# Kernel optimization log

Hardware: AMD Instinct MI355X
Metric: run time of the kernel (lower is better)

## Reference

```python
import jax, jax.numpy as jnp
import numpy as np

N, E, H, HEADS, NC, BLK = 100000, 1600000, 128, 4, 8192, 128

def _layernorm(x, g, b, eps=1e-5):
    m = jnp.mean(x, axis=-1, keepdims=True)
    v = jnp.var(x, axis=-1, keepdims=True)
    return (x - m) * jax.lax.rsqrt(v + eps) * g + b

def setup_inputs() -> dict:
    key = jax.random.key(0)
    ks = jax.random.split(key, 24)
    s = 0.05
    p = lambda k, shp: jax.random.normal(k, shp, jnp.float32) * s
    return {
        'x': jax.random.normal(ks[0], (N, H), jnp.float32),
        'ea': jax.random.normal(ks[1], (E, H), jnp.float32),
        # GINEConv edge linear (edge_dim -> hidden)
        'We': p(ks[2], (H, H)), 'be_': p(ks[3], (H,)),
        # GINEConv mlp: Linear(H,H) -> ReLU -> Linear(H,H)
        'W1': p(ks[4], (H, H)), 'b1': p(ks[5], (H,)),
        'W2': p(ks[6], (H, H)), 'b2': p(ks[7], (H,)),
        'ln1_g': jnp.ones((H,), jnp.float32), 'ln1_b': jnp.zeros((H,), jnp.float32),
        # MultiheadAttention packed qkv + out proj
        'in_w': p(ks[8], (3 * H, H)), 'in_b': p(ks[9], (3 * H,)),
        'out_w': p(ks[10], (H, H)), 'out_b': p(ks[11], (H,)),
        'ln2_g': jnp.ones((H,), jnp.float32), 'ln2_b': jnp.zeros((H,), jnp.float32),
        # FFN: Linear(H,2H) -> ReLU -> Linear(2H,H)
        'f1_w': p(ks[12], (2 * H, H)), 'f1_b': p(ks[13], (2 * H,)),
        'f2_w': p(ks[14], (H, 2 * H)), 'f2_b': p(ks[15], (H,)),
        'ei': jax.random.randint(ks[16], (2, E), 0, N, jnp.int64),
        'chem_idx': jnp.arange(NC, dtype=jnp.int64),
        'B': BLK,
    }

def reference(x, ea, We, be_, W1, b1, W2, b2, ln1_g, ln1_b, in_w, in_b,
              out_w, out_b, ln2_g, ln2_b, f1_w, f1_b, f2_w, f2_b,
              ei, chem_idx, B):
    n = x.shape[0]
    # ---- GINEConv: out_i = mlp((1+eps)*x_i + sum_j relu(x_j + lin(e_ji))), eps=0 ----
    src, dst = ei[0], ei[1]
    msg = jax.nn.relu(x[src] + ea @ We.T + be_)          # [E, H]
    agg = jax.ops.segment_sum(msg, dst, num_segments=n)  # [N, H]
    h = agg + x
    h = jax.nn.relu(h @ W1.T + b1) @ W2.T + b2
    x = _layernorm(x + h, ln1_g, ln1_b)
    # ---- chunked self-attention over chem nodes (chunks of size B) ----
    xc = x[chem_idx].reshape(-1, B, x.shape[-1])         # [nc, B, H]
    nc, _, hid = xc.shape
    dh = hid // HEADS
    qkv = xc @ in_w.T + in_b                             # [nc, B, 3H]
    q, k, v = jnp.split(qkv, 3, axis=-1)
    sp = lambda t: t.reshape(nc, B, HEADS, dh)
    att = jax.nn.softmax(jnp.einsum('bqhd,bkhd->bhqk', sp(q), sp(k)) * (1.0 / np.sqrt(dh)).astype(np.float32), axis=-1)
    o = jnp.einsum('bhqk,bkhd->bqhd', att, sp(v)).reshape(nc, B, hid)
    xc = xc + (o @ out_w.T + out_b)                      # residual inside BlockMHA
    xc = xc.reshape(-1, hid)
    # ---- FFN on chem subset ----
    h2 = _layernorm(xc, ln2_g, ln2_b)
    xc = xc + (jax.nn.relu(h2 @ f1_w.T + f1_b) @ f2_w.T + f2_b)
    return x.at[chem_idx].set(xc)
```

## Files before the change

### kernel.cpp

```cpp
#include <hip/hip_runtime.h>
#include <hip/hip_bf16.h>
#include <math.h>

typedef __attribute__((ext_vector_type(8))) __bf16 bf16x8;
typedef __attribute__((ext_vector_type(4))) float f32x4;
typedef __attribute__((ext_vector_type(4))) unsigned short u16x4;

#define HD  128
#define LDP 136

__device__ __forceinline__ unsigned short f2bf(float f) {
  __bf16 h = (__bf16)f;
  union { __bf16 h; unsigned short u; } v; v.h = h; return v.u;
}
__device__ __forceinline__ float bf2f(unsigned short h) {
  union { unsigned u; float f; } v; v.u = ((unsigned)h) << 16; return v.f;
}

__device__ __forceinline__ int idx_at(const void* p, long long i, int is64) {
  if (is64) return (int)((const long long*)p)[i];
  return ((const int*)p)[i];
}

__device__ __forceinline__ void mfma_tile_128(const unsigned short* a_s,
                                              const unsigned short* w_s,
                                              int w, int l15, int lg,
                                              f32x4 acc[2][8]) {
#pragma unroll
  for (int kk = 0; kk < 4; ++kk) {
    bf16x8 a[2], b[8];
#pragma unroll
    for (int mt = 0; mt < 2; ++mt)
      a[mt] = *(const bf16x8*)&a_s[(w * 32 + mt * 16 + l15) * LDP + kk * 32 + lg * 8];
#pragma unroll
    for (int nt = 0; nt < 8; ++nt)
      b[nt] = *(const bf16x8*)&w_s[(nt * 16 + l15) * LDP + kk * 32 + lg * 8];
#pragma unroll
    for (int mt = 0; mt < 2; ++mt)
#pragma unroll
      for (int nt = 0; nt < 8; ++nt)
        acc[mt][nt] = __builtin_amdgcn_mfma_f32_16x16x32_bf16(a[mt], b[nt], acc[mt][nt], 0, 0, 0);
  }
}

__device__ __forceinline__ void stage_f32(unsigned short* dst, const float* src,
                                          long long src_ld, int tid) {
  for (int i = tid; i < 128 * 32; i += 256) {
    int r = i >> 5, c = (i & 31) << 2;
    float4 f = *(const float4*)&src[(long long)r * src_ld + c];
    u16x4 h = { f2bf(f.x), f2bf(f.y), f2bf(f.z), f2bf(f.w) };
    *(u16x4*)&dst[r * LDP + c] = h;
  }
}

__global__ void detect_idx_kernel(const void* __restrict__ ei, int E, int N,
                                  int* __restrict__ flag) {
  if (threadIdx.x == 0 && blockIdx.x == 0) {
    const long long* p = (const long long*)ei;
    int is64 = 1;
    long long step = E / 64; if (step < 1) step = 1;
    for (int i = 0; i < 64; ++i) {
      long long v = p[i * step];
      if (v < 0 || v >= N) { is64 = 0; break; }
    }
    *flag = is64;
  }
}

__global__ __launch_bounds__(256) void hist_kernel(const void* __restrict__ ei,
                                                   const int* __restrict__ flag,
                                                   int* __restrict__ deg, int E) {
  const int is64 = *flag;
  for (long long e = blockIdx.x * 256LL + threadIdx.x; e < E;
       e += (long long)gridDim.x * 256)
    atomicAdd(&deg[idx_at(ei, (long long)E + e, is64)], 1);
}

#define SCH 1024
__global__ __launch_bounds__(256) void scan_a(const int* __restrict__ deg,
                                              int* __restrict__ bsum, int N) {
  const int b = blockIdx.x, t = threadIdx.x;
  int p = 0;
#pragma unroll
  for (int k = 0; k < 4; ++k) {
    int idx = b * SCH + t * 4 + k;
    if (idx < N) p += deg[idx];
  }
  __shared__ int warr[4];
  for (int o = 32; o > 0; o >>= 1) p += __shfl_xor(p, o);
  if ((t & 63) == 0) warr[t >> 6] = p;
  __syncthreads();
  if (t == 0) bsum[b] = warr[0] + warr[1] + warr[2] + warr[3];
}
__global__ void scan_b(int* __restrict__ bsum, int* __restrict__ off, int NB, int N) {
  if (threadIdx.x == 0 && blockIdx.x == 0) {
    int run = 0;
    for (int b = 0; b < NB; ++b) { int t = bsum[b]; bsum[b] = run; run += t; }
    off[N] = run;
  }
}
__global__ __launch_bounds__(256) void scan_c(const int* __restrict__ deg,
                                              const int* __restrict__ bsum,
                                              int* __restrict__ off,
                                              int* __restrict__ cursor, int N) {
  const int b = blockIdx.x, t = threadIdx.x;
  int d[4], s = 0;
#pragma unroll
  for (int k = 0; k < 4; ++k) {
    int idx = b * SCH + t * 4 + k;
    d[k] = (idx < N) ? deg[idx] : 0;
    s += d[k];
  }
  __shared__ int arr[256];
  arr[t] = s;
  __syncthreads();
  for (int stp = 1; stp < 256; stp <<= 1) {
    int v = (t >= stp) ? arr[t - stp] : 0;
    __syncthreads();
    arr[t] += v;
    __syncthreads();
  }
  int base = bsum[b] + arr[t] - s;
  int acc = 0;
#pragma unroll
  for (int k = 0; k < 4; ++k) {
    int idx = b * SCH + t * 4 + k;
    if (idx < N) { off[idx] = base + acc; cursor[idx] = base + acc; }
    acc += d[k];
  }
}

__global__ __launch_bounds__(256, 3) void edge_kernel4(
    const float* __restrict__ x, const float* __restrict__ ea,
    const float* __restrict__ We, const float* __restrict__ be,
    const void* __restrict__ ei, const int* __restrict__ flag,
    int* __restrict__ cursor, unsigned short* __restrict__ msg, int E, int N) {
  __shared__ unsigned short we_s[128 * LDP];
  __shared__ int s_src[128];
  __shared__ int s_pos[128];
  const int tid = threadIdx.x;
  const long long e0 = (long long)blockIdx.x * 128;
  const int is64 = *flag;

  if (tid < 128) {
    long long e = e0 + tid;
    int s = 0, p = 0;
    if (e < E) {
      s = idx_at(ei, e, is64);
      int d = idx_at(ei, (long long)E + e, is64);
      p = atomicAdd(&cursor[d], 1);
    }
    s_src[tid] = s; s_pos[tid] = p;
  }

  const int lane = tid & 63, w = tid >> 6;
  const int l15 = lane & 15, lg = lane >> 4;

  float4 af[2][4][2];
#pragma unroll
  for (int mt = 0; mt < 2; ++mt) {
    long long row = e0 + w * 32 + mt * 16 + l15;
    const float* src = &ea[(row < E ? row : e0) * HD + lg * 8];
#pragma unroll
    for (int kk = 0; kk < 4; ++kk) {
      af[mt][kk][0] = *(const float4*)&src[kk * 32];
      af[mt][kk][1] = *(const float4*)&src[kk * 32 + 4];
    }
  }

  for (int i = tid; i < 128 * 32; i += 256) {
    int r = i >> 5, c = (i & 31) << 2;
    float4 g = *(const float4*)&We[r * HD + c];
    u16x4 hw = { f2bf(g.x), f2bf(g.y), f2bf(g.z), f2bf(g.w) };
    *(u16x4*)&we_s[r * LDP + c] = hw;
  }

  bf16x8 a[2][4];
#pragma unroll
  for (int mt = 0; mt < 2; ++mt)
#pragma unroll
    for (int kk = 0; kk < 4; ++kk) {
      float4 f0 = af[mt][kk][0], f1 = af[mt][kk][1];
      bf16x8 t;
      t[0] = (__bf16)f0.x; t[1] = (__bf16)f0.y; t[2] = (__bf16)f0.z; t[3] = (__bf16)f0.w;
      t[4] = (__bf16)f1.x; t[5] = (__bf16)f1.y; t[6] = (__bf16)f1.z; t[7] = (__bf16)f1.w;
      a[mt][kk] = t;
    }
  __syncthreads();

  f32x4 acc[2][8];
#pragma unroll
  for (int mt = 0; mt < 2; ++mt)
#pragma unroll
    for (int nt = 0; nt < 8; ++nt) acc[mt][nt] = (f32x4){0.f, 0.f, 0.f, 0.f};

#pragma unroll
  for (int kk = 0; kk < 4; ++kk) {
    bf16x8 b[8];
#pragma unroll
    for (int nt = 0; nt < 8; ++nt)
      b[nt] = *(const bf16x8*)&we_s[(nt * 16 + l15) * LDP + kk * 32 + lg * 8];
#pragma unroll
    for (int mt = 0; mt < 2; ++mt)
#pragma unroll
      for (int nt = 0; nt < 8; ++nt)
        acc[mt][nt] = __builtin_amdgcn_mfma_f32_16x16x32_bf16(a[mt][kk], b[nt], acc[mt][nt], 0, 0, 0);
  }

  float bev[8];
#pragma unroll
  for (int nt = 0; nt < 8; ++nt) bev[nt] = be[nt * 16 + l15];
  __syncthreads();

#pragma unroll
  for (int mt = 0; mt < 2; ++mt) {
#pragma unroll
    for (int r = 0; r < 4; ++r) {
      int m = w * 32 + mt * 16 + lg * 4 + r;
      if (e0 + m >= E) continue;
      const float* xrow = x + (size_t)s_src[m] * HD;
#pragma unroll
      for (int nt = 0; nt < 8; ++nt) {
        int n = nt * 16 + l15;
        float val = acc[mt][nt][r] + bev[nt] + xrow[n];
        we_s[m * LDP + n] = f2bf(val > 0.f ? val : 0.f);
      }
    }
  }
  __syncthreads();
  for (int i = tid; i < 128 * 16; i += 256) {
    int r = i >> 4, sg = i & 15;
    if (e0 + r >= E) continue;
    *(float4*)&msg[(size_t)s_pos[r] * 128 + sg * 8] = *(const float4*)&we_s[r * LDP + sg * 8];
  }
}

__global__ __launch_bounds__(256) void node_kernel2(
    const float* __restrict__ x, float* __restrict__ xo,
    const int* __restrict__ off, const unsigned short* __restrict__ msg,
    const float* __restrict__ W1, const float* __restrict__ b1,
    const float* __restrict__ W2, const float* __restrict__ b2,
    const float* __restrict__ g1, const float* __restrict__ bt1, int N) {
  __shared__ char smem[2 * 128 * LDP * 2];
  unsigned short* a_s = (unsigned short*)smem;
  unsigned short* w_s = (unsigned short*)smem + 128 * LDP;
  float* y_s = (float*)smem;
  const int tid = threadIdx.x;
  const long long r0 = (long long)blockIdx.x * 128;

  const int grp = tid >> 4, li = tid & 15;
  for (int r = grp; r < 128; r += 16) {
    long long gr = r0 + r;
    float a8[8] = {0.f, 0.f, 0.f, 0.f, 0.f, 0.f, 0.f, 0.f};
    if (gr < N) {
      float4 x0 = *(const float4*)&x[(size_t)gr * HD + li * 8];
      float4 x1 = *(const float4*)&x[(size_t)gr * HD + li * 8 + 4];
      a8[0] = x0.x; a8[1] = x0.y; a8[2] = x0.z; a8[3] = x0.w;
      a8[4] = x1.x; a8[5] = x1.y; a8[6] = x1.z; a8[7] = x1.w;
      const int j0 = off[gr], j1 = off[gr + 1];
      int j = j0;
      for (; j + 1 < j1; j += 2) {
        const u16x4* p0 = (const u16x4*)&msg[(size_t)j * 128 + li * 8];
        const u16x4* p1 = (const u16x4*)&msg[(size_t)(j + 1) * 128 + li * 8];
        u16x4 v0 = p0[0], v1 = p0[1], v2 = p1[0], v3 = p1[1];
#pragma unroll
        for (int k = 0; k < 4; ++k) {
          a8[k]     += bf2f(v0[k]) + bf2f(v2[k]);
          a8[4 + k] += bf2f(v1[k]) + bf2f(v3[k]);
        }
      }
      if (j < j1) {
        const u16x4* p0 = (const u16x4*)&msg[(size_t)j * 128 + li * 8];
        u16x4 v0 = p0[0], v1 = p0[1];
#pragma unroll
        for (int k = 0; k < 4; ++k) { a8[k] += bf2f(v0[k]); a8[4 + k] += bf2f(v1[k]); }
      }
    }
    u16x4 h0 = { f2bf(a8[0]), f2bf(a8[1]), f2bf(a8[2]), f2bf(a8[3]) };
    u16x4 h1 = { f2bf(a8[4]), f2bf(a8[5]), f2bf(a8[6]), f2bf(a8[7]) };
    *(u16x4*)&a_s[r * LDP + li * 8] = h0;
    *(u16x4*)&a_s[r * LDP + li * 8 + 4] = h1;
  }
  stage_f32(w_s, W1, HD, tid);
  __syncthreads();

  const int lane = tid & 63, w = tid >> 6;
  const int l15 = lane & 15, lg = lane >> 4;
  f32x4 acc[2][8];
#pragma unroll
  for (int mt = 0; mt < 2; ++mt)
#pragma unroll
    for (int nt = 0; nt < 8; ++nt) acc[mt][nt] = (f32x4){0.f, 0.f, 0.f, 0.f};
  mfma_tile_128(a_s, w_s, w, l15, lg, acc);
  __syncthreads();

#pragma unroll
  for (int mt = 0; mt < 2; ++mt)
#pragma unroll
    for (int r = 0; r < 4; ++r) {
      int m = w * 32 + mt * 16 + lg * 4 + r;
#pragma unroll
      for (int nt = 0; nt < 8; ++nt) {
        int n = nt * 16 + l15;
        float t = acc[mt][nt][r] + b1[n];
        a_s[m * LDP + n] = f2bf(t > 0.f ? t : 0.f);
      }
    }
  stage_f32(w_s, W2, HD, tid);
  __syncthreads();

  f32x4 acc2[2][8];
#pragma unroll
  for (int mt = 0; mt < 2; ++mt)
#pragma unroll
    for (int nt = 0; nt < 8; ++nt) acc2[mt][nt] = (f32x4){0.f, 0.f, 0.f, 0.f};
  mfma_tile_128(a_s, w_s, w, l15, lg, acc2);
  __syncthreads();

#pragma unroll
  for (int mt = 0; mt < 2; ++mt)
#pragma unroll
    for (int r = 0; r < 4; ++r) {
      int m = w * 32 + mt * 16 + lg * 4 + r;
      if (r0 + m < N) {
#pragma unroll
        for (int nt = 0; nt < 8; ++nt) {
          int n = nt * 16 + l15;
          y_s[m * 132 + n] = x[(r0 + m) * HD + n] + acc2[mt][nt][r] + b2[n];
        }
      }
    }
  __syncthreads();

  for (int row = w; row < 128; row += 4) {
    if (r0 + row >= N) continue;
    float v1 = y_s[row * 132 + lane], v2 = y_s[row * 132 + 64 + lane];
    float s = v1 + v2, sq = v1 * v1 + v2 * v2;
    for (int o = 32; o > 0; o >>= 1) { s += __shfl_xor(s, o); sq += __shfl_xor(sq, o); }
    float mean = s * (1.f / 128.f);
    float var = sq * (1.f / 128.f) - mean * mean;
    float rs = rsqrtf(var + 1e-5f);
    xo[(r0 + row) * HD + lane]      = (v1 - mean) * rs * g1[lane] + bt1[lane];
    xo[(r0 + row) * HD + 64 + lane] = (v2 - mean) * rs * g1[lane + 64] + bt1[lane + 64];
  }
}

__global__ __launch_bounds__(256) void edge_kernel(
    const float* __restrict__ x, const float* __restrict__ ea,
    const float* __restrict__ We, const float* __restrict__ be,
    const void* __restrict__ ei, const int* __restrict__ flag,
    float* __restrict__ agg, int E, int N) {
  __shared__ unsigned short ea_s[128 * LDP];
  __shared__ unsigned short we_s[128 * LDP];
  __shared__ int s_src[128];
  __shared__ int s_dst[128];
  const int tid = threadIdx.x;
  const long long e0 = (long long)blockIdx.x * 128;
  const int is64 = *flag;
  if (tid < 128) {
    long long e = e0 + tid;
    int s = 0, d = 0;
    if (e < E) { s = idx_at(ei, e, is64); d = idx_at(ei, (long long)E + e, is64); }
    s_src[tid] = s; s_dst[tid] = d;
  }
  for (int i = tid; i < 128 * 32; i += 256) {
    int r = i >> 5, c = (i & 31) << 2;
    float4 f = {0.f, 0.f, 0.f, 0.f};
    if (e0 + r < E) f = *(const float4*)&ea[(e0 + r) * HD + c];
    u16x4 h = { f2bf(f.x), f2bf(f.y), f2bf(f.z), f2bf(f.w) };
    *(u16x4*)&ea_s[r * LDP + c] = h;
    float4 g = *(const float4*)&We[r * HD + c];
    u16x4 hw = { f2bf(g.x), f2bf(g.y), f2bf(g.z), f2bf(g.w) };
    *(u16x4*)&we_s[r * LDP + c] = hw;
  }
  __syncthreads();
  const int lane = tid & 63, w = tid >> 6;
  const int l15 = lane & 15, lg = lane >> 4;
  f32x4 acc[2][8];
#pragma unroll
  for (int mt = 0; mt < 2; ++mt)
#pragma unroll
    for (int nt = 0; nt < 8; ++nt) acc[mt][nt] = (f32x4){0.f, 0.f, 0.f, 0.f};
  mfma_tile_128(ea_s, we_s, w, l15, lg, acc);
  float bev[8];
#pragma unroll
  for (int nt = 0; nt < 8; ++nt) bev[nt] = be[nt * 16 + l15];
#pragma unroll
  for (int mt = 0; mt < 2; ++mt) {
#pragma unroll
    for (int r = 0; r < 4; ++r) {
      int m = w * 32 + mt * 16 + lg * 4 + r;
      if (e0 + m >= E) continue;
      const float* xrow = x + (size_t)s_src[m] * HD;
      float* arow = agg + (size_t)s_dst[m] * HD;
#pragma unroll
      for (int nt = 0; nt < 8; ++nt) {
        int n = nt * 16 + l15;
        float val = acc[mt][nt][r] + bev[nt] + xrow[n];
        if (val > 0.f) unsafeAtomicAdd(&arow[n], val);
      }
    }
  }
}

__global__ __launch_bounds__(256) void node_kernel(
    const float* __restrict__ x, float* xo,
    const float* __restrict__ W1, const float* __restrict__ b1,
    const float* __restrict__ W2, const float* __restrict__ b2,
    const float* __restrict__ g1, const float* __restrict__ bt1, int N) {
  __shared__ char smem[2 * 128 * LDP * 2];
  unsigned short* a_s = (unsigned short*)smem;
  unsigned short* w_s = (unsigned short*)smem + 128 * LDP;
  float* y_s = (float*)smem;
  const int tid = threadIdx.x;
  const long long r0 = (long long)blockIdx.x * 128;
  for (int i = tid; i < 128 * 32; i += 256) {
    int r = i >> 5, c = (i & 31) << 2;
    float4 f = {0.f, 0.f, 0.f, 0.f};
    if (r0 + r < N) {
      float4 xa = *(const float4*)&x[(r0 + r) * HD + c];
      float4 ag = *(const float4*)&xo[(r0 + r) * HD + c];
      f.x = xa.x + ag.x; f.y = xa.y + ag.y; f.z = xa.z + ag.z; f.w = xa.w + ag.w;
    }
    u16x4 h = { f2bf(f.x), f2bf(f.y), f2bf(f.z), f2bf(f.w) };
    *(u16x4*)&a_s[r * LDP + c] = h;
    float4 g = *(const float4*)&W1[r * HD + c];
    u16x4 hw = { f2bf(g.x), f2bf(g.y), f2bf(g.z), f2bf(g.w) };
    *(u16x4*)&w_s[r * LDP + c] = hw;
  }
  __syncthreads();
  const int lane = tid & 63, w = tid >> 6;
  const int l15 = lane & 15, lg = lane >> 4;
  f32x4 acc[2][8];
#pragma unroll
  for (int mt = 0; mt < 2; ++mt)
#pragma unroll
    for (int nt = 0; nt < 8; ++nt) acc[mt][nt] = (f32x4){0.f, 0.f, 0.f, 0.f};
  mfma_tile_128(a_s, w_s, w, l15, lg, acc);
  __syncthreads();
#pragma unroll
  for (int mt = 0; mt < 2; ++mt)
#pragma unroll
    for (int r = 0; r < 4; ++r) {
      int m = w * 32 + mt * 16 + lg * 4 + r;
#pragma unroll
      for (int nt = 0; nt < 8; ++nt) {
        int n = nt * 16 + l15;
        float t = acc[mt][nt][r] + b1[n];
        a_s[m * LDP + n] = f2bf(t > 0.f ? t : 0.f);
      }
    }
  stage_f32(w_s, W2, HD, tid);
  __syncthreads();
  f32x4 acc2[2][8];
#pragma unroll
  for (int mt = 0; mt < 2; ++mt)
#pragma unroll
    for (int nt = 0; nt < 8; ++nt) acc2[mt][nt] = (f32x4){0.f, 0.f, 0.f, 0.f};
  mfma_tile_128(a_s, w_s, w, l15, lg, acc2);
  __syncthreads();
#pragma unroll
  for (int mt = 0; mt < 2; ++mt)
#pragma unroll
    for (int r = 0; r < 4; ++r) {
      int m = w * 32 + mt * 16 + lg * 4 + r;
      if (r0 + m < N) {
#pragma unroll
        for (int nt = 0; nt < 8; ++nt) {
          int n = nt * 16 + l15;
          y_s[m * 132 + n] = x[(r0 + m) * HD + n] + acc2[mt][nt][r] + b2[n];
        }
      }
    }
  __syncthreads();
  for (int row = w; row < 128; row += 4) {
    if (r0 + row >= N) continue;
    float v1 = y_s[row * 132 + lane], v2 = y_s[row * 132 + 64 + lane];
    float s = v1 + v2, sq = v1 * v1 + v2 * v2;
    for (int o = 32; o > 0; o >>= 1) { s += __shfl_xor(s, o); sq += __shfl_xor(sq, o); }
    float mean = s * (1.f / 128.f);
    float var = sq * (1.f / 128.f) - mean * mean;
    float rs = rsqrtf(var + 1e-5f);
    xo[(r0 + row) * HD + lane]      = (v1 - mean) * rs * g1[lane] + bt1[lane];
    xo[(r0 + row) * HD + 64 + lane] = (v2 - mean) * rs * g1[lane + 64] + bt1[lane + 64];
  }
}

__global__ __launch_bounds__(256) void qkv_kernel(
    const float* __restrict__ xo, const float* __restrict__ in_w,
    const float* __restrict__ in_b, const void* __restrict__ chem,
    const int* __restrict__ flag, float* __restrict__ qkv) {
  __shared__ unsigned short a_s[128 * LDP];
  __shared__ unsigned short w_s[128 * LDP];
  __shared__ int s_row[128];
  const int tid = threadIdx.x;
  const int chunk = blockIdx.x, sec = blockIdx.y;
  const int is64 = *flag;
  if (tid < 128) s_row[tid] = idx_at(chem, (long long)chunk * 128 + tid, is64);
  __syncthreads();
  for (int i = tid; i < 128 * 32; i += 256) {
    int r = i >> 5, c = (i & 31) << 2;
    float4 f = *(const float4*)&xo[(size_t)s_row[r] * HD + c];
    u16x4 h = { f2bf(f.x), f2bf(f.y), f2bf(f.z), f2bf(f.w) };
    *(u16x4*)&a_s[r * LDP + c] = h;
    float4 g = *(const float4*)&in_w[(size_t)(sec * 128 + r) * HD + c];
    u16x4 hw = { f2bf(g.x), f2bf(g.y), f2bf(g.z), f2bf(g.w) };
    *(u16x4*)&w_s[r * LDP + c] = hw;
  }
  __syncthreads();
  const int lane = tid & 63, w = tid >> 6;
  const int l15 = lane & 15, lg = lane >> 4;
  f32x4 acc[2][8];
#pragma unroll
  for (int mt = 0; mt < 2; ++mt)
#pragma unroll
    for (int nt = 0; nt < 8; ++nt) acc[mt][nt] = (f32x4){0.f, 0.f, 0.f, 0.f};
  mfma_tile_128(a_s, w_s, w, l15, lg, acc);
#pragma unroll
  for (int mt = 0; mt < 2; ++mt)
#pragma unroll
    for (int r = 0; r < 4; ++r) {
      int m = w * 32 + mt * 16 + lg * 4 + r;
#pragma unroll
      for (int nt = 0; nt < 8; ++nt) {
        int n = nt * 16 + l15;
        qkv[(size_t)(chunk * 128 + m) * 384 + sec * 128 + n] = acc[mt][nt][r] + in_b[sec * 128 + n];
      }
    }
}

__global__ __launch_bounds__(128) void attn_kernel(const float* __restrict__ qkv,
                                                   float* __restrict__ o) {
  __shared__ float k_s[128 * 32];
  __shared__ float v_s[128 * 32];
  const int tid = threadIdx.x;
  const int chunk = blockIdx.x, h = blockIdx.y;
  const float scale = 0.1767766952966369f;
  for (int i = tid; i < 128 * 32; i += 128) {
    int r = i >> 5, d = i & 31;
    k_s[i] = qkv[(size_t)(chunk * 128 + r) * 384 + 128 + h * 32 + d];
    v_s[i] = qkv[(size_t)(chunk * 128 + r) * 384 + 256 + h * 32 + d];
  }
  float qr[32];
  const int m = tid;
#pragma unroll
  for (int d = 0; d < 32; ++d)
    qr[d] = qkv[(size_t)(chunk * 128 + m) * 384 + h * 32 + d] * scale;
  __syncthreads();
  float mx = -1e30f, sm = 0.f;
  for (int j = 0; j < 128; ++j) {
    float s = 0.f;
#pragma unroll
    for (int d = 0; d < 32; ++d) s += qr[d] * k_s[j * 32 + d];
    if (s > mx) { sm = sm * __expf(mx - s); mx = s; }
    sm += __expf(s - mx);
  }
  const float inv = 1.f / sm;
  float ov[32];
#pragma unroll
  for (int d = 0; d < 32; ++d) ov[d] = 0.f;
  for (int j = 0; j < 128; ++j) {
    float s = 0.f;
#pragma unroll
    for (int d = 0; d < 32; ++d) s += qr[d] * k_s[j * 32 + d];
    float p = __expf(s - mx) * inv;
#pragma unroll
    for (int d = 0; d < 32; ++d) ov[d] += p * v_s[j * 32 + d];
  }
#pragma unroll
  for (int d = 0; d < 32; ++d)
    o[(size_t)(chunk * 128 + m) * HD + h * 32 + d] = ov[d];
}

__global__ __launch_bounds__(256) void oproj_kernel(
    const float* __restrict__ xo, const float* __restrict__ o,
    const float* __restrict__ Wo, const float* __restrict__ bo,
    const float* __restrict__ g2, const float* __restrict__ bt2,
    const void* __restrict__ chem, const int* __restrict__ flag,
    float* __restrict__ xc2, unsigned short* __restrict__ h2b) {
  __shared__ char smem[2 * 128 * LDP * 2];
  unsigned short* a_s = (unsigned short*)smem;
  unsigned short* w_s = (unsigned short*)smem + 128 * LDP;
  float* y_s = (float*)smem;
  __shared__ int s_row[128];
  const int tid = threadIdx.x;
  const int chunk = blockIdx.x;
  const int is64 = *flag;
  if (tid < 128) s_row[tid] = idx_at(chem, (long long)chunk * 128 + tid, is64);
  stage_f32(a_s, o + (size_t)chunk * 128 * HD, HD, tid);
  stage_f32(w_s, Wo, HD, tid);
  __syncthreads();
  const int lane = tid & 63, w = tid >> 6;
  const int l15 = lane & 15, lg = lane >> 4;
  f32x4 acc[2][8];
#pragma unroll
  for (int mt = 0; mt < 2; ++mt)
#pragma unroll
    for (int nt = 0; nt < 8; ++nt) acc[mt][nt] = (f32x4){0.f, 0.f, 0.f, 0.f};
  mfma_tile_128(a_s, w_s, w, l15, lg, acc);
  __syncthreads();
#pragma unroll
  for (int mt = 0; mt < 2; ++mt)
#pragma unroll
    for (int r = 0; r < 4; ++r) {
      int m = w * 32 + mt * 16 + lg * 4 + r;
#pragma unroll
      for (int nt = 0; nt < 8; ++nt) {
        int n = nt * 16 + l15;
        y_s[m * 132 + n] = xo[(size_t)s_row[m] * HD + n] + acc[mt][nt][r] + bo[n];
      }
    }
  __syncthreads();
  for (int row = w; row < 128; row += 4) {
    float v1 = y_s[row * 132 + lane], v2 = y_s[row * 132 + 64 + lane];
    float s = v1 + v2, sq = v1 * v1 + v2 * v2;
    for (int o2 = 32; o2 > 0; o2 >>= 1) { s += __shfl_xor(s, o2); sq += __shfl_xor(sq, o2); }
    float mean = s * (1.f / 128.f);
    float var = sq * (1.f / 128.f) - mean * mean;
    float rs = rsqrtf(var + 1e-5f);
    size_t gi = (size_t)(chunk * 128 + row) * HD;
    xc2[gi + lane] = v1; xc2[gi + 64 + lane] = v2;
    h2b[gi + lane]      = f2bf((v1 - mean) * rs * g2[lane] + bt2[lane]);
    h2b[gi + 64 + lane] = f2bf((v2 - mean) * rs * g2[lane + 64] + bt2[lane + 64]);
  }
}

__global__ __launch_bounds__(256) void ffn1_kernel(
    const unsigned short* __restrict__ h2b, const float* __restrict__ f1w,
    const float* __restrict__ f1b, unsigned short* __restrict__ u) {
  __shared__ unsigned short a_s[128 * LDP];
  __shared__ unsigned short w_s[128 * LDP];
  const int tid = threadIdx.x;
  const int chunk = blockIdx.x, sec = blockIdx.y;
  for (int i = tid; i < 128 * 32; i += 256) {
    int r = i >> 5, c = (i & 31) << 2;
    *(u16x4*)&a_s[r * LDP + c] = *(const u16x4*)&h2b[(size_t)(chunk * 128 + r) * HD + c];
  }
  stage_f32(w_s, f1w + (size_t)sec * 128 * HD, HD, tid);
  __syncthreads();
  const int lane = tid & 63, w = tid >> 6;
  const int l15 = lane & 15, lg = lane >> 4;
  f32x4 acc[2][8];
#pragma unroll
  for (int mt = 0; mt < 2; ++mt)
#pragma unroll
    for (int nt = 0; nt < 8; ++nt) acc[mt][nt] = (f32x4){0.f, 0.f, 0.f, 0.f};
  mfma_tile_128(a_s, w_s, w, l15, lg, acc);
#pragma unroll
  for (int mt = 0; mt < 2; ++mt)
#pragma unroll
    for (int r = 0; r < 4; ++r) {
      int m = w * 32 + mt * 16 + lg * 4 + r;
#pragma unroll
      for (int nt = 0; nt < 8; ++nt) {
        int n = nt * 16 + l15;
        float t = acc[mt][nt][r] + f1b[sec * 128 + n];
        u[(size_t)(chunk * 128 + m) * 256 + sec * 128 + n] = f2bf(t > 0.f ? t : 0.f);
      }
    }
}

__global__ __launch_bounds__(256) void ffn2_kernel(
    const unsigned short* __restrict__ u, const float* __restrict__ f2w,
    const float* __restrict__ f2b, const float* __restrict__ xc2,
    const void* __restrict__ chem, const int* __restrict__ flag,
    float* __restrict__ out) {
  __shared__ unsigned short a_s[128 * LDP];
  __shared__ unsigned short w_s[128 * LDP];
  __shared__ int s_row[128];
  const int tid = threadIdx.x;
  const int chunk = blockIdx.x;
  const int is64 = *flag;
  if (tid < 128) s_row[tid] = idx_at(chem, (long long)chunk * 128 + tid, is64);
  const int lane = tid & 63, w = tid >> 6;
  const int l15 = lane & 15, lg = lane >> 4;
  f32x4 acc[2][8];
#pragma unroll
  for (int mt = 0; mt < 2; ++mt)
#pragma unroll
    for (int nt = 0; nt < 8; ++nt) acc[mt][nt] = (f32x4){0.f, 0.f, 0.f, 0.f};
  for (int half = 0; half < 2; ++half) {
    __syncthreads();
    for (int i = tid; i < 128 * 32; i += 256) {
      int r = i >> 5, c = (i & 31) << 2;
      *(u16x4*)&a_s[r * LDP + c] =
          *(const u16x4*)&u[(size_t)(chunk * 128 + r) * 256 + half * 128 + c];
      float4 g = *(const float4*)&f2w[(size_t)r * 256 + half * 128 + c];
      u16x4 hw = { f2bf(g.x), f2bf(g.y), f2bf(g.z), f2bf(g.w) };
      *(u16x4*)&w_s[r * LDP + c] = hw;
    }
    __syncthreads();
    mfma_tile_128(a_s, w_s, w, l15, lg, acc);
  }
#pragma unroll
  for (int mt = 0; mt < 2; ++mt)
#pragma unroll
    for (int r = 0; r < 4; ++r) {
      int m = w * 32 + mt * 16 + lg * 4 + r;
#pragma unroll
      for (int nt = 0; nt < 8; ++nt) {
        int n = nt * 16 + l15;
        float val = xc2[(size_t)(chunk * 128 + m) * HD + n] + acc[mt][nt][r] + f2b[n];
        out[(size_t)s_row[m] * HD + n] = val;
      }
    }
}

extern "C" void kernel_launch(void* const* d_in, const int* in_sizes, int n_in,
                              void* d_out, int out_size, void* d_ws, size_t ws_size,
                              hipStream_t stream) {
  const float* x    = (const float*)d_in[0];
  const float* ea   = (const float*)d_in[1];
  const float* We   = (const float*)d_in[2];
  const float* be   = (const float*)d_in[3];
  const float* W1   = (const float*)d_in[4];
  const float* b1   = (const float*)d_in[5];
  const float* W2   = (const float*)d_in[6];
  const float* b2   = (const float*)d_in[7];
  const float* g1   = (const float*)d_in[8];
  const float* bt1  = (const float*)d_in[9];
  const float* in_w = (const float*)d_in[10];
  const float* in_b = (const float*)d_in[11];
  const float* outw = (const float*)d_in[12];
  const float* outb = (const float*)d_in[13];
  const float* g2   = (const float*)d_in[14];
  const float* bt2  = (const float*)d_in[15];
  const float* f1w  = (const float*)d_in[16];
  const float* f1b  = (const float*)d_in[17];
  const float* f2w  = (const float*)d_in[18];
  const float* f2b  = (const float*)d_in[19];
  const void*  ei   = d_in[20];
  const void*  chem = d_in[21];
  const int N  = in_sizes[0] / HD;
  const int E  = in_sizes[1] / HD;
  const int NC = in_sizes[21];
  const int NB = (N + SCH - 1) / SCH;
  float* xo = (float*)d_out;

  char* ws = (char*)d_ws;
  size_t o = 0;
  auto alloc = [&](size_t bytes) { size_t p = o; o = (o + bytes + 255) & ~255ULL; return p; };
  size_t o_qkv  = alloc((size_t)NC * 384 * 4);
  size_t o_obuf = alloc((size_t)NC * 128 * 4);
  size_t o_xc2  = alloc((size_t)NC * 128 * 4);
  size_t o_h2b  = alloc((size_t)NC * 128 * 2);
  size_t o_ubuf = alloc((size_t)NC * 256 * 2);
  size_t o_flag = alloc(4);
  size_t o_deg  = alloc((size_t)N * 4);
  size_t o_off  = alloc((size_t)(N + 1) * 4);
  size_t o_cur  = alloc((size_t)N * 4);
  size_t o_bsum = alloc((size_t)NB * 4);
  size_t o_msg  = alloc((size_t)E * 128 * 2);
  size_t need = o;

  float*          qkv  = (float*)(ws + o_qkv);
  float*          obuf = (float*)(ws + o_obuf);
  float*          xc2  = (float*)(ws + o_xc2);
  unsigned short* h2b  = (unsigned short*)(ws + o_h2b);
  unsigned short* ubuf = (unsigned short*)(ws + o_ubuf);
  int*            flag = (int*)(ws + o_flag);
  int*            deg  = (int*)(ws + o_deg);
  int*            off  = (int*)(ws + o_off);
  int*            cur  = (int*)(ws + o_cur);
  int*            bsum = (int*)(ws + o_bsum);
  unsigned short* msg  = (unsigned short*)(ws + o_msg);

  detect_idx_kernel<<<1, 64, 0, stream>>>(ei, E, N, flag);

  if (ws_size >= need) {
    hipMemsetAsync(deg, 0, (size_t)N * 4, stream);
    hist_kernel<<<dim3(1024), 256, 0, stream>>>(ei, flag, deg, E);
    scan_a<<<dim3(NB), 256, 0, stream>>>(deg, bsum, N);
    scan_b<<<1, 64, 0, stream>>>(bsum, off, NB, N);
    scan_c<<<dim3(NB), 256, 0, stream>>>(deg, bsum, off, cur, N);
    edge_kernel4<<<dim3((E + 127) / 128), 256, 0, stream>>>(x, ea, We, be, ei, flag,
                                                            cur, msg, E, N);
    node_kernel2<<<dim3((N + 127) / 128), 256, 0, stream>>>(x, xo, off, msg, W1, b1,
                                                            W2, b2, g1, bt1, N);
  } else {
    hipMemsetAsync(xo, 0, (size_t)N * HD * sizeof(float), stream);
    edge_kernel<<<dim3((E + 127) / 128), 256, 0, stream>>>(x, ea, We, be, ei, flag, xo, E, N);
    node_kernel<<<dim3((N + 127) / 128), 256, 0, stream>>>(x, xo, W1, b1, W2, b2, g1, bt1, N);
  }

  const int ncs = NC / 128;
  qkv_kernel<<<dim3(ncs, 3), 256, 0, stream>>>(xo, in_w, in_b, chem, flag, qkv);
  attn_kernel<<<dim3(ncs, 4), 128, 0, stream>>>(qkv, obuf);
  oproj_kernel<<<dim3(ncs), 256, 0, stream>>>(xo, obuf, outw, outb, g2, bt2, chem, flag, xc2, h2b);
  ffn1_kernel<<<dim3(ncs, 2), 256, 0, stream>>>(h2b, f1w, f1b, ubuf);
  ffn2_kernel<<<dim3(ncs), 256, 0, stream>>>(ubuf, f2w, f2b, xc2, chem, flag, xo);
}
```

Baseline: 807.4 us.

## Replace bf16 message buffer with dst-sorted edge ids and segmented atomic aggregation

Removes the large per-edge bf16 message buffer and the CSR gather in node_kernel2. A new scatter kernel writes edge ids and destinations in destination-sorted order. The edge kernel then processes edges in that order and sums consecutive same-destination rows in registers before issuing float atomics into the aggregation buffer, which node_kernel then consumes. This avoids writing and re-reading the E x 128 message array, at the cost of gathered (non-contiguous) ea row reads, an extra scatter pass, and float atomics that make the summation order nondeterministic.

```diff
diff --git a/kernel.cpp b/kernel.cpp
--- a/kernel.cpp
+++ b/kernel.cpp
@@ -130,27 +130,41 @@
   }
 }
 
-__global__ __launch_bounds__(256, 3) void edge_kernel4(
+__global__ __launch_bounds__(256) void scatter_eid_kernel(
+    const void* __restrict__ ei, const int* __restrict__ flag,
+    int* __restrict__ cursor, int* __restrict__ eid, int* __restrict__ dstc, int E) {
+  const int is64 = *flag;
+  for (long long e = blockIdx.x * 256LL + threadIdx.x; e < E;
+       e += (long long)gridDim.x * 256) {
+    int d = idx_at(ei, (long long)E + e, is64);
+    int pos = atomicAdd(&cursor[d], 1);
+    eid[pos] = (int)e;
+    dstc[pos] = d;
+  }
+}
+
+__global__ __launch_bounds__(256, 3) void edge_kernel5(
     const float* __restrict__ x, const float* __restrict__ ea,
     const float* __restrict__ We, const float* __restrict__ be,
     const void* __restrict__ ei, const int* __restrict__ flag,
-    int* __restrict__ cursor, unsigned short* __restrict__ msg, int E, int N) {
+    const int* __restrict__ eid, const int* __restrict__ dstc,
+    float* __restrict__ agg, int E) {
   __shared__ unsigned short we_s[128 * LDP];
   __shared__ int s_src[128];
-  __shared__ int s_pos[128];
+  __shared__ int s_dst[128];
   const int tid = threadIdx.x;
-  const long long e0 = (long long)blockIdx.x * 128;
+  const long long j0 = (long long)blockIdx.x * 128;
   const int is64 = *flag;
 
   if (tid < 128) {
-    long long e = e0 + tid;
-    int s = 0, p = 0;
-    if (e < E) {
-      s = idx_at(ei, e, is64);
-      int d = idx_at(ei, (long long)E + e, is64);
-      p = atomicAdd(&cursor[d], 1);
-    }
-    s_src[tid] = s; s_pos[tid] = p;
+    long long j = j0 + tid;
+    int srcv = 0, d = -1;
+    if (j < E) {
+      int e = eid[j];
+      srcv = idx_at(ei, e, is64);
+      d = dstc[j];
+    }
+    s_src[tid] = srcv; s_dst[tid] = d;
   }
 
   const int lane = tid & 63, w = tid >> 6;
@@ -159,8 +173,9 @@
   float4 af[2][4][2];
 #pragma unroll
   for (int mt = 0; mt < 2; ++mt) {
-    long long row = e0 + w * 32 + mt * 16 + l15;
-    const float* src = &ea[(row < E ? row : e0) * HD + lg * 8];
+    long long j = j0 + w * 32 + mt * 16 + l15;
+    int e = (j < E) ? eid[j] : 0;
+    const float* src = &ea[(size_t)e * HD + lg * 8];
 #pragma unroll
     for (int kk = 0; kk < 4; ++kk) {
       af[mt][kk][0] = *(const float4*)&src[kk * 32];
@@ -210,138 +225,42 @@
   float bev[8];
 #pragma unroll
   for (int nt = 0; nt < 8; ++nt) bev[nt] = be[nt * 16 + l15];
-  __syncthreads();
 
 #pragma unroll
   for (int mt = 0; mt < 2; ++mt) {
+    const int mbase = w * 32 + mt * 16 + lg * 4;
+    float vsum[8];
+    int cur = -1;
 #pragma unroll
     for (int r = 0; r < 4; ++r) {
-      int m = w * 32 + mt * 16 + lg * 4 + r;
-      if (e0 + m >= E) continue;
-      const float* xrow = x + (size_t)s_src[m] * HD;
-#pragma unroll
-      for (int nt = 0; nt < 8; ++nt) {
-        int n = nt * 16 + l15;
-        float val = acc[mt][nt][r] + bev[nt] + xrow[n];
-        we_s[m * LDP + n] = f2bf(val > 0.f ? val : 0.f);
-      }
-    }
-  }
-  __syncthreads();
-  for (int i = tid; i < 128 * 16; i += 256) {
-    int r = i >> 4, sg = i & 15;
-    if (e0 + r >= E) continue;
-    *(float4*)&msg[(size_t)s_pos[r] * 128 + sg * 8] = *(const float4*)&we_s[r * LDP + sg * 8];
-  }
-}
-
-__global__ __launch_bounds__(256) void node_kernel2(
-    const float* __restrict__ x, float* __restrict__ xo,
-    const int* __restrict__ off, const unsigned short* __restrict__ msg,
-    const float* __restrict__ W1, const float* __restrict__ b1,
-    const float* __restrict__ W2, const float* __restrict__ b2,
-    const float* __restrict__ g1, const float* __restrict__ bt1, int N) {
-  __shared__ char smem[2 * 128 * LDP * 2];
-  unsigned short* a_s = (unsigned short*)smem;
-  unsigned short* w_s = (unsigned short*)smem + 128 * LDP;
-  float* y_s = (float*)smem;
-  const int tid = threadIdx.x;
-  const long long r0 = (long long)blockIdx.x * 128;
-
-  const int grp = tid >> 4, li = tid & 15;
-  for (int r = grp; r < 128; r += 16) {
-    long long gr = r0 + r;
-    float a8[8] = {0.f, 0.f, 0.f, 0.f, 0.f, 0.f, 0.f, 0.f};
-    if (gr < N) {
-      float4 x0 = *(const float4*)&x[(size_t)gr * HD + li * 8];
-      float4 x1 = *(const float4*)&x[(size_t)gr * HD + li * 8 + 4];
-      a8[0] = x0.x; a8[1] = x0.y; a8[2] = x0.z; a8[3] = x0.w;
-      a8[4] = x1.x; a8[5] = x1.y; a8[6] = x1.z; a8[7] = x1.w;
-      const int j0 = off[gr], j1 = off[gr + 1];
-      int j = j0;
-      for (; j + 1 < j1; j += 2) {
-        const u16x4* p0 = (const u16x4*)&msg[(size_t)j * 128 + li * 8];
-        const u16x4* p1 = (const u16x4*)&msg[(size_t)(j + 1) * 128 + li * 8];
-        u16x4 v0 = p0[0], v1 = p0[1], v2 = p1[0], v3 = p1[1];
-#pragma unroll
-        for (int k = 0; k < 4; ++k) {
-          a8[k]     += bf2f(v0[k]) + bf2f(v2[k]);
-          a8[4 + k] += bf2f(v1[k]) + bf2f(v3[k]);
+      const int m = mbase + r;
+      const int d = s_dst[m];
+      if (d != cur) {
+        if (cur >= 0) {
+          float* arow = agg + (size_t)cur * HD;
+#pragma unroll
+          for (int nt = 0; nt < 8; ++nt)
+            if (vsum[nt] > 0.f) unsafeAtomicAdd(&arow[nt * 16 + l15], vsum[nt]);
         }
-      }
-      if (j < j1) {
-        const u16x4* p0 = (const u16x4*)&msg[(size_t)j * 128 + li * 8];
-        u16x4 v0 = p0[0], v1 = p0[1];
-#pragma unroll
-        for (int k = 0; k < 4; ++k) { a8[k] += bf2f(v0[k]); a8[4 + k] += bf2f(v1[k]); }
-      }
-    }
-    u16x4 h0 = { f2bf(a8[0]), f2bf(a8[1]), f2bf(a8[2]), f2bf(a8[3]) };
-    u16x4 h1 = { f2bf(a8[4]), f2bf(a8[5]), f2bf(a8[6]), f2bf(a8[7]) };
-    *(u16x4*)&a_s[r * LDP + li * 8] = h0;
-    *(u16x4*)&a_s[r * LDP + li * 8 + 4] = h1;
-  }
-  stage_f32(w_s, W1, HD, tid);
-  __syncthreads();
-
-  const int lane = tid & 63, w = tid >> 6;
-  const int l15 = lane & 15, lg = lane >> 4;
-  f32x4 acc[2][8];
-#pragma unroll
-  for (int mt = 0; mt < 2; ++mt)
-#pragma unroll
-    for (int nt = 0; nt < 8; ++nt) acc[mt][nt] = (f32x4){0.f, 0.f, 0.f, 0.f};
-  mfma_tile_128(a_s, w_s, w, l15, lg, acc);
-  __syncthreads();
-
-#pragma unroll
-  for (int mt = 0; mt < 2; ++mt)
-#pragma unroll
-    for (int r = 0; r < 4; ++r) {
-      int m = w * 32 + mt * 16 + lg * 4 + r;
-#pragma unroll
-      for (int nt = 0; nt < 8; ++nt) {
-        int n = nt * 16 + l15;
-        float t = acc[mt][nt][r] + b1[n];
-        a_s[m * LDP + n] = f2bf(t > 0.f ? t : 0.f);
-      }
-    }
-  stage_f32(w_s, W2, HD, tid);
-  __syncthreads();
-
-  f32x4 acc2[2][8];
-#pragma unroll
-  for (int mt = 0; mt < 2; ++mt)
-#pragma unroll
-    for (int nt = 0; nt < 8; ++nt) acc2[mt][nt] = (f32x4){0.f, 0.f, 0.f, 0.f};
-  mfma_tile_128(a_s, w_s, w, l15, lg, acc2);
-  __syncthreads();
-
-#pragma unroll
-  for (int mt = 0; mt < 2; ++mt)
-#pragma unroll
-    for (int r = 0; r < 4; ++r) {
-      int m = w * 32 + mt * 16 + lg * 4 + r;
-      if (r0 + m < N) {
+        cur = d;
+#pragma unroll
+        for (int nt = 0; nt < 8; ++nt) vsum[nt] = 0.f;
+      }
+      if (d >= 0) {
+        const float* xrow = x + (size_t)s_src[m] * HD;
 #pragma unroll
         for (int nt = 0; nt < 8; ++nt) {
-          int n = nt * 16 + l15;
-          y_s[m * 132 + n] = x[(r0 + m) * HD + n] + acc2[mt][nt][r] + b2[n];
+          float val = acc[mt][nt][r] + bev[nt] + xrow[nt * 16 + l15];
+          vsum[nt] += (val > 0.f ? val : 0.f);
         }
       }
     }
-  __syncthreads();
-
-  for (int row = w; row < 128; row += 4) {
-    if (r0 + row >= N) continue;
-    float v1 = y_s[row * 132 + lane], v2 = y_s[row * 132 + 64 + lane];
-    float s = v1 + v2, sq = v1 * v1 + v2 * v2;
-    for (int o = 32; o > 0; o >>= 1) { s += __shfl_xor(s, o); sq += __shfl_xor(sq, o); }
-    float mean = s * (1.f / 128.f);
-    float var = sq * (1.f / 128.f) - mean * mean;
-    float rs = rsqrtf(var + 1e-5f);
-    xo[(r0 + row) * HD + lane]      = (v1 - mean) * rs * g1[lane] + bt1[lane];
-    xo[(r0 + row) * HD + 64 + lane] = (v2 - mean) * rs * g1[lane + 64] + bt1[lane + 64];
+    if (cur >= 0) {
+      float* arow = agg + (size_t)cur * HD;
+#pragma unroll
+      for (int nt = 0; nt < 8; ++nt)
+        if (vsum[nt] > 0.f) unsafeAtomicAdd(&arow[nt * 16 + l15], vsum[nt]);
+    }
   }
 }
 
@@ -750,7 +669,8 @@
   size_t o_off  = alloc((size_t)(N + 1) * 4);
   size_t o_cur  = alloc((size_t)N * 4);
   size_t o_bsum = alloc((size_t)NB * 4);
-  size_t o_msg  = alloc((size_t)E * 128 * 2);
+  size_t o_eid  = alloc((size_t)E * 4);
+  size_t o_dstc = alloc((size_t)E * 4);
   size_t need = o;
 
   float*          qkv  = (float*)(ws + o_qkv);
@@ -763,9 +683,11 @@
   int*            off  = (int*)(ws + o_off);
   int*            cur  = (int*)(ws + o_cur);
   int*            bsum = (int*)(ws + o_bsum);
-  unsigned short* msg  = (unsigned short*)(ws + o_msg);
+  int*            eid  = (int*)(ws + o_eid);
+  int*            dstc = (int*)(ws + o_dstc);
 
   detect_idx_kernel<<<1, 64, 0, stream>>>(ei, E, N, flag);
+  hipMemsetAsync(xo, 0, (size_t)N * HD * sizeof(float), stream);
 
   if (ws_size >= need) {
     hipMemsetAsync(deg, 0, (size_t)N * 4, stream);
@@ -773,15 +695,13 @@
     scan_a<<<dim3(NB), 256, 0, stream>>>(deg, bsum, N);
     scan_b<<<1, 64, 0, stream>>>(bsum, off, NB, N);
     scan_c<<<dim3(NB), 256, 0, stream>>>(deg, bsum, off, cur, N);
-    edge_kernel4<<<dim3((E + 127) / 128), 256, 0, stream>>>(x, ea, We, be, ei, flag,
-                                                            cur, msg, E, N);
-    node_kernel2<<<dim3((N + 127) / 128), 256, 0, stream>>>(x, xo, off, msg, W1, b1,
-                                                            W2, b2, g1, bt1, N);
+    scatter_eid_kernel<<<dim3(1024), 256, 0, stream>>>(ei, flag, cur, eid, dstc, E);
+    edge_kernel5<<<dim3((E + 127) / 128), 256, 0, stream>>>(x, ea, We, be, ei, flag,
+                                                            eid, dstc, xo, E);
   } else {
-    hipMemsetAsync(xo, 0, (size_t)N * HD * sizeof(float), stream);
     edge_kernel<<<dim3((E + 127) / 128), 256, 0, stream>>>(x, ea, We, be, ei, flag, xo, E, N);
-    node_kernel<<<dim3((N + 127) / 128), 256, 0, stream>>>(x, xo, W1, b1, W2, b2, g1, bt1, N);
-  }
+  }
+  node_kernel<<<dim3((N + 127) / 128), 256, 0, stream>>>(x, xo, W1, b1, W2, b2, g1, bt1, N);
 
   const int ncs = NC / 128;
   qkv_kernel<<<dim3(ncs, 3), 256, 0, stream>>>(xo, in_w, in_b, chem, flag, qkv);
```

Measured after the change: 1.103 ms. +36.5%, slower.

## Aggregate node messages via flat edge-parallel LDS atomics with precomputed bf16 We

Applied to the files above, without the earlier changes.

The edge kernel now records the destination of each sorted edge slot. The node kernel (512 threads) then walks the block's contiguous message range flat and accumulates into an LDS fp32 tile with shared atomics, which removes the load imbalance of the per-row segmented loops. We is converted to bf16 once by a small pre-kernel, so each edge block copies it instead of converting it again, and edge kernel occupancy is raised to 4. In exchange this adds LDS atomic contention, an extra E-sized index buffer to write and read, and half of the node threads sit idle during the MFMA phases.

```diff
diff --git a/kernel.cpp b/kernel.cpp
--- a/kernel.cpp
+++ b/kernel.cpp
@@ -43,9 +43,9 @@
   }
 }
 
-__device__ __forceinline__ void stage_f32(unsigned short* dst, const float* src,
-                                          long long src_ld, int tid) {
-  for (int i = tid; i < 128 * 32; i += 256) {
+__device__ __forceinline__ void stage_f32s(unsigned short* dst, const float* src,
+                                           long long src_ld, int tid, int T) {
+  for (int i = tid; i < 128 * 32; i += T) {
     int r = i >> 5, c = (i & 31) << 2;
     float4 f = *(const float4*)&src[(long long)r * src_ld + c];
     u16x4 h = { f2bf(f.x), f2bf(f.y), f2bf(f.z), f2bf(f.w) };
@@ -67,6 +67,15 @@
   }
 }
 
+__global__ __launch_bounds__(256) void conv_we_kernel(const float* __restrict__ We,
+                                                      unsigned short* __restrict__ we_bf) {
+  int i = blockIdx.x * 256 + threadIdx.x;
+  if (i < 128 * 128) {
+    int r = i >> 7, c = i & 127;
+    we_bf[r * 136 + c] = f2bf(We[i]);
+  }
+}
+
 __global__ __launch_bounds__(256) void hist_kernel(const void* __restrict__ ei,
                                                    const int* __restrict__ flag,
                                                    int* __restrict__ deg, int E) {
@@ -130,11 +139,12 @@
   }
 }
 
-__global__ __launch_bounds__(256, 3) void edge_kernel4(
+__global__ __launch_bounds__(256, 4) void edge_kernel6(
     const float* __restrict__ x, const float* __restrict__ ea,
-    const float* __restrict__ We, const float* __restrict__ be,
+    const unsigned short* __restrict__ we_bf, const float* __restrict__ be,
     const void* __restrict__ ei, const int* __restrict__ flag,
-    int* __restrict__ cursor, unsigned short* __restrict__ msg, int E, int N) {
+    int* __restrict__ cursor, int* __restrict__ dstc,
+    unsigned short* __restrict__ msg, int E) {
   __shared__ unsigned short we_s[128 * LDP];
   __shared__ int s_src[128];
   __shared__ int s_pos[128];
@@ -149,6 +159,7 @@
       s = idx_at(ei, e, is64);
       int d = idx_at(ei, (long long)E + e, is64);
       p = atomicAdd(&cursor[d], 1);
+      dstc[p] = d;
     }
     s_src[tid] = s; s_pos[tid] = p;
   }
@@ -168,11 +179,9 @@
     }
   }
 
-  for (int i = tid; i < 128 * 32; i += 256) {
-    int r = i >> 5, c = (i & 31) << 2;
-    float4 g = *(const float4*)&We[r * HD + c];
-    u16x4 hw = { f2bf(g.x), f2bf(g.y), f2bf(g.z), f2bf(g.w) };
-    *(u16x4*)&we_s[r * LDP + c] = hw;
+  for (int i = tid; i < 2048; i += 256) {
+    int r = i >> 4, c = (i & 15) << 3;
+    *(float4*)&we_s[r * LDP + c] = *(const float4*)&we_bf[r * 136 + c];
   }
 
   bf16x8 a[2][4];
@@ -235,53 +244,71 @@
   }
 }
 
-__global__ __launch_bounds__(256) void node_kernel2(
+#define NNT 512
+__global__ __launch_bounds__(NNT, 1) void node_kernel6(
     const float* __restrict__ x, float* __restrict__ xo,
-    const int* __restrict__ off, const unsigned short* __restrict__ msg,
+    const int* __restrict__ off, const int* __restrict__ dstc,
+    const unsigned short* __restrict__ msg,
     const float* __restrict__ W1, const float* __restrict__ b1,
     const float* __restrict__ W2, const float* __restrict__ b2,
     const float* __restrict__ g1, const float* __restrict__ bt1, int N) {
+  __shared__ float agg_s[128 * 132];
   __shared__ char smem[2 * 128 * LDP * 2];
   unsigned short* a_s = (unsigned short*)smem;
   unsigned short* w_s = (unsigned short*)smem + 128 * LDP;
   float* y_s = (float*)smem;
   const int tid = threadIdx.x;
   const long long r0 = (long long)blockIdx.x * 128;
-
+  const int rows = (N - r0 < 128) ? (int)(N - r0) : 128;
+
+  for (int i = tid; i < 128 * 132; i += NNT) agg_s[i] = 0.f;
+  __syncthreads();
+
+  const int jlo = off[r0];
+  const int jhi = off[r0 + rows];
   const int grp = tid >> 4, li = tid & 15;
-  for (int r = grp; r < 128; r += 16) {
-    long long gr = r0 + r;
-    float a8[8] = {0.f, 0.f, 0.f, 0.f, 0.f, 0.f, 0.f, 0.f};
-    if (gr < N) {
-      float4 x0 = *(const float4*)&x[(size_t)gr * HD + li * 8];
-      float4 x1 = *(const float4*)&x[(size_t)gr * HD + li * 8 + 4];
-      a8[0] = x0.x; a8[1] = x0.y; a8[2] = x0.z; a8[3] = x0.w;
-      a8[4] = x1.x; a8[5] = x1.y; a8[6] = x1.z; a8[7] = x1.w;
-      const int j0 = off[gr], j1 = off[gr + 1];
-      int j = j0;
-      for (; j + 1 < j1; j += 2) {
-        const u16x4* p0 = (const u16x4*)&msg[(size_t)j * 128 + li * 8];
-        const u16x4* p1 = (const u16x4*)&msg[(size_t)(j + 1) * 128 + li * 8];
-        u16x4 v0 = p0[0], v1 = p0[1], v2 = p1[0], v3 = p1[1];
-#pragma unroll
-        for (int k = 0; k < 4; ++k) {
-          a8[k]     += bf2f(v0[k]) + bf2f(v2[k]);
-          a8[4 + k] += bf2f(v1[k]) + bf2f(v3[k]);
-        }
-      }
-      if (j < j1) {
-        const u16x4* p0 = (const u16x4*)&msg[(size_t)j * 128 + li * 8];
-        u16x4 v0 = p0[0], v1 = p0[1];
-#pragma unroll
-        for (int k = 0; k < 4; ++k) { a8[k] += bf2f(v0[k]); a8[4 + k] += bf2f(v1[k]); }
-      }
-    }
-    u16x4 h0 = { f2bf(a8[0]), f2bf(a8[1]), f2bf(a8[2]), f2bf(a8[3]) };
-    u16x4 h1 = { f2bf(a8[4]), f2bf(a8[5]), f2bf(a8[6]), f2bf(a8[7]) };
-    *(u16x4*)&a_s[r * LDP + li * 8] = h0;
-    *(u16x4*)&a_s[r * LDP + li * 8 + 4] = h1;
-  }
-  stage_f32(w_s, W1, HD, tid);
+  const int co = li * 8;
+  int j = jlo + grp;
+  for (; j + 32 < jhi; j += 64) {
+    int d0 = dstc[j] - (int)r0;
+    int d1 = dstc[j + 32] - (int)r0;
+    const u16x4* p0 = (const u16x4*)&msg[(size_t)j * 128 + co];
+    const u16x4* p1 = (const u16x4*)&msg[(size_t)(j + 32) * 128 + co];
+    u16x4 v0 = p0[0], v1 = p0[1], v2 = p1[0], v3 = p1[1];
+    float* q0 = &agg_s[d0 * 132 + co];
+    float* q1 = &agg_s[d1 * 132 + co];
+#pragma unroll
+    for (int k = 0; k < 4; ++k) {
+      atomicAdd(&q0[k], bf2f(v0[k])); atomicAdd(&q0[4 + k], bf2f(v1[k]));
+      atomicAdd(&q1[k], bf2f(v2[k])); atomicAdd(&q1[4 + k], bf2f(v3[k]));
+    }
+  }
+  if (j < jhi) {
+    int d0 = dstc[j] - (int)r0;
+    const u16x4* p0 = (const u16x4*)&msg[(size_t)j * 128 + co];
+    u16x4 v0 = p0[0], v1 = p0[1];
+    float* q0 = &agg_s[d0 * 132 + co];
+#pragma unroll
+    for (int k = 0; k < 4; ++k) {
+      atomicAdd(&q0[k], bf2f(v0[k])); atomicAdd(&q0[4 + k], bf2f(v1[k]));
+    }
+  }
+  __syncthreads();
+
+  for (int i = tid; i < 128 * 32; i += NNT) {
+    int r = i >> 5, c = (i & 31) << 2;
+    float4 f = {0.f, 0.f, 0.f, 0.f};
+    if (r < rows) {
+      float4 xa = *(const float4*)&x[(r0 + r) * HD + c];
+      f.x = xa.x + agg_s[r * 132 + c];
+      f.y = xa.y + agg_s[r * 132 + c + 1];
+      f.z = xa.z + agg_s[r * 132 + c + 2];
+      f.w = xa.w + agg_s[r * 132 + c + 3];
+    }
+    u16x4 h = { f2bf(f.x), f2bf(f.y), f2bf(f.z), f2bf(f.w) };
+    *(u16x4*)&a_s[r * LDP + c] = h;
+  }
+  stage_f32s(w_s, W1, HD, tid, NNT);
   __syncthreads();
 
   const int lane = tid & 63, w = tid >> 6;
@@ -291,49 +318,53 @@
   for (int mt = 0; mt < 2; ++mt)
 #pragma unroll
     for (int nt = 0; nt < 8; ++nt) acc[mt][nt] = (f32x4){0.f, 0.f, 0.f, 0.f};
-  mfma_tile_128(a_s, w_s, w, l15, lg, acc);
-  __syncthreads();
-
-#pragma unroll
-  for (int mt = 0; mt < 2; ++mt)
-#pragma unroll
-    for (int r = 0; r < 4; ++r) {
-      int m = w * 32 + mt * 16 + lg * 4 + r;
-#pragma unroll
-      for (int nt = 0; nt < 8; ++nt) {
-        int n = nt * 16 + l15;
-        float t = acc[mt][nt][r] + b1[n];
-        a_s[m * LDP + n] = f2bf(t > 0.f ? t : 0.f);
-      }
-    }
-  stage_f32(w_s, W2, HD, tid);
-  __syncthreads();
-
-  f32x4 acc2[2][8];
-#pragma unroll
-  for (int mt = 0; mt < 2; ++mt)
-#pragma unroll
-    for (int nt = 0; nt < 8; ++nt) acc2[mt][nt] = (f32x4){0.f, 0.f, 0.f, 0.f};
-  mfma_tile_128(a_s, w_s, w, l15, lg, acc2);
-  __syncthreads();
-
-#pragma unroll
-  for (int mt = 0; mt < 2; ++mt)
-#pragma unroll
-    for (int r = 0; r < 4; ++r) {
-      int m = w * 32 + mt * 16 + lg * 4 + r;
-      if (r0 + m < N) {
+  if (tid < 256) mfma_tile_128(a_s, w_s, w, l15, lg, acc);
+  __syncthreads();
+
+  if (tid < 256) {
+#pragma unroll
+    for (int mt = 0; mt < 2; ++mt)
+#pragma unroll
+      for (int r = 0; r < 4; ++r) {
+        int m = w * 32 + mt * 16 + lg * 4 + r;
 #pragma unroll
         for (int nt = 0; nt < 8; ++nt) {
           int n = nt * 16 + l15;
-          y_s[m * 132 + n] = x[(r0 + m) * HD + n] + acc2[mt][nt][r] + b2[n];
+          float t = acc[mt][nt][r] + b1[n];
+          a_s[m * LDP + n] = f2bf(t > 0.f ? t : 0.f);
         }
       }
-    }
-  __syncthreads();
-
-  for (int row = w; row < 128; row += 4) {
-    if (r0 + row >= N) continue;
+  }
+  stage_f32s(w_s, W2, HD, tid, NNT);
+  __syncthreads();
+
+  f32x4 acc2[2][8];
+#pragma unroll
+  for (int mt = 0; mt < 2; ++mt)
+#pragma unroll
+    for (int nt = 0; nt < 8; ++nt) acc2[mt][nt] = (f32x4){0.f, 0.f, 0.f, 0.f};
+  if (tid < 256) mfma_tile_128(a_s, w_s, w, l15, lg, acc2);
+  __syncthreads();
+
+  if (tid < 256) {
+#pragma unroll
+    for (int mt = 0; mt < 2; ++mt)
+#pragma unroll
+      for (int r = 0; r < 4; ++r) {
+        int m = w * 32 + mt * 16 + lg * 4 + r;
+        if (r0 + m < N) {
+#pragma unroll
+          for (int nt = 0; nt < 8; ++nt) {
+            int n = nt * 16 + l15;
+            y_s[m * 132 + n] = x[(r0 + m) * HD + n] + acc2[mt][nt][r] + b2[n];
+          }
+        }
+      }
+  }
+  __syncthreads();
+
+  const int w8 = tid >> 6;
+  for (int row = w8; row < rows; row += 8) {
     float v1 = y_s[row * 132 + lane], v2 = y_s[row * 132 + 64 + lane];
     float s = v1 + v2, sq = v1 * v1 + v2 * v2;
     for (int o = 32; o > 0; o >>= 1) { s += __shfl_xor(s, o); sq += __shfl_xor(sq, o); }
@@ -450,7 +481,7 @@
         a_s[m * LDP + n] = f2bf(t > 0.f ? t : 0.f);
       }
     }
-  stage_f32(w_s, W2, HD, tid);
+  stage_f32s(w_s, W2, HD, tid, 256);
   __syncthreads();
   f32x4 acc2[2][8];
 #pragma unroll
@@ -587,8 +618,8 @@
   const int chunk = blockIdx.x;
   const int is64 = *flag;
   if (tid < 128) s_row[tid] = idx_at(chem, (long long)chunk * 128 + tid, is64);
-  stage_f32(a_s, o + (size_t)chunk * 128 * HD, HD, tid);
-  stage_f32(w_s, Wo, HD, tid);
+  stage_f32s(a_s, o + (size_t)chunk * 128 * HD, HD, tid, 256);
+  stage_f32s(w_s, Wo, HD, tid, 256);
   __syncthreads();
   const int lane = tid & 63, w = tid >> 6;
   const int l15 = lane & 15, lg = lane >> 4;
@@ -636,7 +667,7 @@
     int r = i >> 5, c = (i & 31) << 2;
     *(u16x4*)&a_s[r * LDP + c] = *(const u16x4*)&h2b[(size_t)(chunk * 128 + r) * HD + c];
   }
-  stage_f32(w_s, f1w + (size_t)sec * 128 * HD, HD, tid);
+  stage_f32s(w_s, f1w + (size_t)sec * 128 * HD, HD, tid, 256);
   __syncthreads();
   const int lane = tid & 63, w = tid >> 6;
   const int l15 = lane & 15, lg = lane >> 4;
@@ -746,10 +777,12 @@
   size_t o_h2b  = alloc((size_t)NC * 128 * 2);
   size_t o_ubuf = alloc((size_t)NC * 256 * 2);
   size_t o_flag = alloc(4);
+  size_t o_webf = alloc(128 * 136 * 2);
   size_t o_deg  = alloc((size_t)N * 4);
   size_t o_off  = alloc((size_t)(N + 1) * 4);
   size_t o_cur  = alloc((size_t)N * 4);
   size_t o_bsum = alloc((size_t)NB * 4);
+  size_t o_dstc = alloc((size_t)E * 4);
   size_t o_msg  = alloc((size_t)E * 128 * 2);
   size_t need = o;
 
@@ -759,10 +792,12 @@
   unsigned short* h2b  = (unsigned short*)(ws + o_h2b);
   unsigned short* ubuf = (unsigned short*)(ws + o_ubuf);
   int*            flag = (int*)(ws + o_flag);
+  unsigned short* webf = (unsigned short*)(ws + o_webf);
   int*            deg  = (int*)(ws + o_deg);
   int*            off  = (int*)(ws + o_off);
   int*            cur  = (int*)(ws + o_cur);
   int*            bsum = (int*)(ws + o_bsum);
+  int*            dstc = (int*)(ws + o_dstc);
   unsigned short* msg  = (unsigned short*)(ws + o_msg);
 
   detect_idx_kernel<<<1, 64, 0, stream>>>(ei, E, N, flag);
@@ -773,10 +808,11 @@
     scan_a<<<dim3(NB), 256, 0, stream>>>(deg, bsum, N);
     scan_b<<<1, 64, 0, stream>>>(bsum, off, NB, N);
     scan_c<<<dim3(NB), 256, 0, stream>>>(deg, bsum, off, cur, N);
-    edge_kernel4<<<dim3((E + 127) / 128), 256, 0, stream>>>(x, ea, We, be, ei, flag,
-                                                            cur, msg, E, N);
-    node_kernel2<<<dim3((N + 127) / 128), 256, 0, stream>>>(x, xo, off, msg, W1, b1,
-                                                            W2, b2, g1, bt1, N);
+    conv_we_kernel<<<dim3(64), 256, 0, stream>>>(We, webf);
+    edge_kernel6<<<dim3((E + 127) / 128), 256, 0, stream>>>(x, ea, webf, be, ei, flag,
+                                                            cur, dstc, msg, E);
+    node_kernel6<<<dim3((N + 127) / 128), NNT, 0, stream>>>(x, xo, off, dstc, msg, W1,
+                                                            b1, W2, b2, g1, bt1, N);
   } else {
     hipMemsetAsync(xo, 0, (size_t)N * HD * sizeof(float), stream);
     edge_kernel<<<dim3((E + 127) / 128), 256, 0, stream>>>(x, ea, We, be, ei, flag, xo, E, N);
```

After: 2.006 ms. +148.4%, slower.
